# Optimization experiments

Hardware: AMD Instinct MI355X
Metric: run time of the kernel (lower is better)

## Reference

```python
import jax, jax.numpy as jnp
import numpy as np

H = 512          # hidden_size
L = 1024         # total sequence length (q_len + c_len + t_len)
C = 512          # number of columns (key/value length)
NUM_REL = 51     # len(relations2id)


def setup_inputs() -> dict:
    key = jax.random.key(0)
    ks = jax.random.split(key, 12)
    w = 1.0 / np.sqrt(H)  # torch nn.Linear default init scale
    return {
        "query": jax.random.normal(ks[0], (1, L, H), jnp.float32),
        "key": jax.random.normal(ks[1], (1, C, H), jnp.float32),
        "value": jax.random.normal(ks[2], (1, C, H), jnp.float32),
        "predefined_relation": jax.random.randint(ks[3], (L, L), 0, NUM_REL, dtype=jnp.int32),
        "q_len": 384,
        "c_len": 512,
        "Wq": jax.random.uniform(ks[4], (H, H), jnp.float32, -w, w),
        "bq": jnp.zeros((H,), jnp.float32),
        "Wk": jax.random.uniform(ks[5], (H, H), jnp.float32, -w, w),
        "bk": jnp.zeros((H,), jnp.float32),
        "Wv": jax.random.uniform(ks[6], (H, H), jnp.float32, -w, w),
        "bv": jnp.zeros((H,), jnp.float32),
        "rel_k_emb": jax.random.normal(ks[7], (NUM_REL, H), jnp.float32),
        "rel_v_emb": jax.random.normal(ks[8], (NUM_REL, H), jnp.float32),
    }


def reference(query, key, value, predefined_relation, q_len, c_len,
              Wq, bq, Wk, bk, Wv, bv, rel_k_emb, rel_v_emb):
    # --- get_fixed_column_relation (kind='column', enable_latent_relations=False) ---
    # predefined_relation: [L, L] relation ids; take column block [L, C]
    mc = predefined_relation[:, q_len:q_len + c_len]          # [L, C]
    relation_k = rel_k_emb[mc]                                # [L, C, H]
    relation_v = rel_v_emb[mc]                                # [L, C, H] (value path discarded by forward)
    # --- single-head projections (nbatches == 1) ---
    q = query[0] @ Wq.T + bq                                  # [L, H]
    k = key[0] @ Wk.T + bk                                    # [C, H]
    v = value[0] @ Wv.T + bv                                  # [C, H]
    # --- relative_attention_logits ---
    qk = q @ k.T                                              # [L, C]
    q_rel = jnp.einsum('lh,lch->lc', q, relation_k)           # per-query relation scores [L, C]
    scores = (qk + q_rel) / np.sqrt(H).astype(np.float32)
    attn = jax.nn.softmax(scores, axis=-1)                    # [L, C]
    # forward returns self.attn[0, 0] (the pre-dropout attention probabilities);
    # relative_attention_values output (attn @ v + einsum('lc,lch->lh', attn, relation_v))
    # is computed in the torch module but discarded, so we return only attn.
    return attn
```

## Files before the change

### kernel.cpp

```cpp
#include <hip/hip_runtime.h>
#include <hip/hip_bf16.h>

#define HH 512
#define LL 1024
#define CC 512
#define NREL 51

typedef __attribute__((ext_vector_type(8))) short bf16x8;
typedef __attribute__((ext_vector_type(4))) float f32x4;
typedef __attribute__((ext_vector_type(2))) float f32x2;

__device__ __forceinline__ short f2bn(float f) {
    return __builtin_bit_cast(short, __float2bfloat16(f));
}

__device__ __forceinline__ void gl16(const void* g, void* l) {
    __builtin_amdgcn_global_load_lds(
        (const __attribute__((address_space(1))) void*)g,
        (__attribute__((address_space(3))) void*)l, 16, 0, 0);
}

__global__ __launch_bounds__(256) void k1_proj(
    const float* __restrict__ query, const float* __restrict__ key,
    const float* __restrict__ Wq, const float* __restrict__ Wk,
    const float* __restrict__ relk, const float* __restrict__ bq,
    short* __restrict__ qbuf, short* __restrict__ kbuf,
    float* __restrict__ Rpart)
{
    __shared__ __align__(16) short Alds[16 * 512];
    __shared__ __align__(16) short Blds[64 * 512];
    const int b = blockIdx.x, tid = threadIdx.x;
    const int w = tid >> 6, lane = tid & 63;
    const bool isq = (b < 512);
    const float *A, *B; short* outp; int m0, n0;
    if (isq) { A = query; B = Wq; outp = qbuf;
               m0 = (b >> 3) * 16; n0 = (b & 7) * 64; }
    else     { const int bb = b - 512; A = key; B = Wk; outp = kbuf;
               m0 = (bb >> 3) * 16; n0 = (bb & 7) * 64; }

    {
        const int ar = tid >> 4, ac = (tid & 15) * 8;
        #pragma unroll
        for (int j = 0; j < 4; ++j) {
            const int c = ac + j * 128;
            float4 x = *(const float4*)(A + (m0 + ar) * HH + c);
            float4 y = *(const float4*)(A + (m0 + ar) * HH + c + 4);
            bf16x8 o;
            o[0] = f2bn(x.x); o[1] = f2bn(x.y); o[2] = f2bn(x.z); o[3] = f2bn(x.w);
            o[4] = f2bn(y.x); o[5] = f2bn(y.y); o[6] = f2bn(y.z); o[7] = f2bn(y.w);
            *(bf16x8*)(Alds + ar * 512 + (((c >> 3) ^ (ar & 7)) << 3)) = o;
        }
        const int br = tid >> 2, bc = (tid & 3) * 16;
        #pragma unroll
        for (int j = 0; j < 8; ++j) {
            const int c = bc + j * 64;
            float4 x0 = *(const float4*)(B + (n0 + br) * HH + c);
            float4 x1 = *(const float4*)(B + (n0 + br) * HH + c + 4);
            float4 x2 = *(const float4*)(B + (n0 + br) * HH + c + 8);
            float4 x3 = *(const float4*)(B + (n0 + br) * HH + c + 12);
            bf16x8 o0, o1;
            o0[0] = f2bn(x0.x); o0[1] = f2bn(x0.y); o0[2] = f2bn(x0.z); o0[3] = f2bn(x0.w);
            o0[4] = f2bn(x1.x); o0[5] = f2bn(x1.y); o0[6] = f2bn(x1.z); o0[7] = f2bn(x1.w);
            o1[0] = f2bn(x2.x); o1[1] = f2bn(x2.y); o1[2] = f2bn(x2.z); o1[3] = f2bn(x2.w);
            o1[4] = f2bn(x3.x); o1[5] = f2bn(x3.y); o1[6] = f2bn(x3.z); o1[7] = f2bn(x3.w);
            *(bf16x8*)(Blds + br * 512 + ((((c >> 3) + 0) ^ (br & 7)) << 3)) = o0;
            *(bf16x8*)(Blds + br * 512 + ((((c >> 3) + 1) ^ (br & 7)) << 3)) = o1;
        }
    }
    __syncthreads();

    const int lr = lane & 15, lk = (lane >> 4) * 8;
    const int lx = 8 * (lr & 7);
    f32x4 acc[4] = {};
    #pragma unroll
    for (int t = 0; t < 2; ++t) {
        const int k0g = w * 128 + t * 64;
        bf16x8 a0 = *(const bf16x8*)(Alds + lr * 512 + k0g + ((0 + lk) ^ lx));
        bf16x8 a1 = *(const bf16x8*)(Alds + lr * 512 + k0g + ((32 + lk) ^ lx));
        #pragma unroll
        for (int f = 0; f < 4; ++f) {
            const int ro = (f * 16 + lr) * 512 + k0g;
            bf16x8 b0 = *(const bf16x8*)(Blds + ro + ((0 + lk) ^ lx));
            bf16x8 b1 = *(const bf16x8*)(Blds + ro + ((32 + lk) ^ lx));
            acc[f] = __builtin_amdgcn_mfma_f32_16x16x32_bf16(a0, b0, acc[f], 0, 0, 0);
            acc[f] = __builtin_amdgcn_mfma_f32_16x16x32_bf16(a1, b1, acc[f], 0, 0, 0);
        }
    }
    __syncthreads();

    float* P = (float*)Blds;
    if (w) {
        #pragma unroll
        for (int f = 0; f < 4; ++f)
            *(f32x4*)(P + (w - 1) * 1024 + lane * 16 + f * 4) = acc[f];
    }
    __syncthreads();

    short* qt   = Blds + 8192;
    short* Brel = Blds + 16384;
    if (w == 0) {
        #pragma unroll
        for (int wv = 0; wv < 3; ++wv)
            #pragma unroll
            for (int f = 0; f < 4; ++f)
                acc[f] += *(const f32x4*)(P + wv * 1024 + lane * 16 + f * 4);
        #pragma unroll
        for (int f = 0; f < 4; ++f) {
            const int colg = f * 16 + lr;
            const float bv = isq ? bq[n0 + colg] : 0.f;
            #pragma unroll
            for (int r = 0; r < 4; ++r) {
                const int row = (lane >> 4) * 4 + r;
                const short h = f2bn(acc[f][r] + bv);
                outp[(m0 + row) * HH + n0 + (colg ^ (8 * (row & 7)))] = h;
                if (isq)
                    qt[row * 64 + (((colg >> 3) ^ (row & 7)) << 3) + (colg & 7)] = h;
            }
        }
    } else if (isq) {
        for (int i = tid - 64; i < 1024; i += 192) {
            const int rr = i >> 4, c4 = (i & 15) * 4;
            float4 v = make_float4(0.f, 0.f, 0.f, 0.f);
            if (rr < NREL) v = *(const float4*)(relk + rr * HH + n0 + c4);
            short4 o;
            o.x = f2bn(v.x); o.y = f2bn(v.y); o.z = f2bn(v.z); o.w = f2bn(v.w);
            *(short4*)(Brel + rr * 64 + (((c4 >> 3) ^ (rr & 7)) << 3) + (c4 & 7)) = o;
        }
    }
    __syncthreads();

    if (w == 0 && isq) {
        bf16x8 a0 = *(const bf16x8*)(qt + lr * 64 + ((0 + lk) ^ lx));
        bf16x8 a1 = *(const bf16x8*)(qt + lr * 64 + ((32 + lk) ^ lx));
        f32x4 racc[4] = {};
        #pragma unroll
        for (int f = 0; f < 4; ++f) {
            const int ro = (f * 16 + lr) * 64;
            bf16x8 b0 = *(const bf16x8*)(Brel + ro + ((0 + lk) ^ lx));
            bf16x8 b1 = *(const bf16x8*)(Brel + ro + ((32 + lk) ^ lx));
            racc[f] = __builtin_amdgcn_mfma_f32_16x16x32_bf16(a0, b0, racc[f], 0, 0, 0);
            racc[f] = __builtin_amdgcn_mfma_f32_16x16x32_bf16(a1, b1, racc[f], 0, 0, 0);
        }
        #pragma unroll
        for (int f = 0; f < 4; ++f)
            #pragma unroll
            for (int r = 0; r < 4; ++r)
                Rpart[(b & 7) * (LL * 64) + (m0 + (lane >> 4) * 4 + r) * 64 + f * 16 + lr]
                    = racc[f][r];
    }
}

__global__ __launch_bounds__(512) void k2_attn(
    const short* __restrict__ qbuf, const short* __restrict__ kbuf,
    const int* __restrict__ rel, const int* __restrict__ qlen,
    const float* __restrict__ Rpart, float* __restrict__ out)
{
    __shared__ __align__(16) short Bb[8][2][4096];
    __shared__ float Rs[16][64];
    __shared__ float psum[8][16];
    const int b = blockIdx.x, tid = threadIdx.x;
    const int w = tid >> 6, lane = tid & 63;
    const int l0 = b * 16, cb = w * 64;
    const int lr = lane & 15, lk = (lane >> 4) * 8;
    const int lx = 8 * (lr & 7);
    const int srow = lane >> 3, scol = (lane & 7) * 8;
    const int qoff = qlen[0];

    const int rrow = tid >> 5, rc = (tid & 31) * 2;
    f32x2 rpv[8];
    #pragma unroll
    for (int p = 0; p < 8; ++p)
        rpv[p] = *(const f32x2*)(Rpart + p * (LL * 64) + (l0 + rrow) * 64 + rc);
    int idxr[4][4];
    #pragma unroll
    for (int r = 0; r < 4; ++r) {
        const int row = (lane >> 4) * 4 + r;
        #pragma unroll
        for (int f = 0; f < 4; ++f)
            idxr[r][f] = rel[(l0 + row) * LL + qoff + cb + f * 16 + lr];
    }
    __builtin_amdgcn_sched_barrier(0);

    bf16x8 a0v[2], a1v[2];
#define K2_STAGE(bi, t) do { \
        const int k0g = (t) * 64; \
        short* Lb = &Bb[w][bi][0]; \
        _Pragma("unroll") \
        for (int j = 0; j < 8; ++j) \
            gl16(kbuf + (cb + j * 8 + srow) * HH + k0g + scol, Lb + j * 512); \
        a0v[bi] = *(const bf16x8*)(qbuf + (l0 + lr) * HH + k0g + ((0 + lk) ^ lx)); \
        a1v[bi] = *(const bf16x8*)(qbuf + (l0 + lr) * HH + k0g + ((32 + lk) ^ lx)); \
    } while (0)

    f32x4 acc[4] = {};
#define K2_COMP(bi) do { \
        const short* Lb = &Bb[w][bi][0]; \
        _Pragma("unroll") \
        for (int f = 0; f < 4; ++f) { \
            const int ro = (f * 16 + lr) * 64; \
            bf16x8 k0f = *(const bf16x8*)(Lb + ro + ((0 + lk) ^ lx)); \
            bf16x8 k1f = *(const bf16x8*)(Lb + ro + ((32 + lk) ^ lx)); \
            acc[f] = __builtin_amdgcn_mfma_f32_16x16x32_bf16(a0v[bi], k0f, acc[f], 0, 0, 0); \
            acc[f] = __builtin_amdgcn_mfma_f32_16x16x32_bf16(a1v[bi], k1f, acc[f], 0, 0, 0); \
        } \
    } while (0)

    K2_STAGE(0, 0);
    #pragma unroll
    for (int t = 0; t < 8; ++t) {
        if (t < 7) {
            K2_STAGE((t + 1) & 1, t + 1);
            asm volatile("s_waitcnt vmcnt(10)" ::: "memory");
        } else {
            asm volatile("s_waitcnt vmcnt(0)" ::: "memory");
        }
        __builtin_amdgcn_sched_barrier(0);
        K2_COMP(t & 1);
    }
#undef K2_STAGE
#undef K2_COMP

    float rx = 0.f, ry = 0.f;
    #pragma unroll
    for (int p = 0; p < 8; ++p) { rx += rpv[p][0]; ry += rpv[p][1]; }
    Rs[rrow][rc] = rx; Rs[rrow][rc + 1] = ry;
    __syncthreads();

    const float scale = 0.04419417382415922f;
    #pragma unroll
    for (int r = 0; r < 4; ++r) {
        const int row = (lane >> 4) * 4 + r;
        float s = 0.f;
        #pragma unroll
        for (int f = 0; f < 4; ++f) {
            float e = __expf((acc[f][r] + Rs[row][idxr[r][f]]) * scale);
            acc[f][r] = e; s += e;
        }
        #pragma unroll
        for (int sh = 1; sh < 16; sh <<= 1) s += __shfl_xor(s, sh, 64);
        if (lr == 0) psum[w][row] = s;
    }
    __syncthreads();
    #pragma unroll
    for (int r = 0; r < 4; ++r) {
        const int row = (lane >> 4) * 4 + r;
        float tot = 0.f;
        #pragma unroll
        for (int wv = 0; wv < 8; ++wv) tot += psum[wv][row];
        const float inv = 1.f / tot;
        #pragma unroll
        for (int f = 0; f < 4; ++f)
            out[(l0 + row) * CC + cb + f * 16 + lr] = acc[f][r] * inv;
    }
}

extern "C" void kernel_launch(void* const* d_in, const int* in_sizes, int n_in,
                              void* d_out, int out_size, void* d_ws, size_t ws_size,
                              hipStream_t stream) {
    const float* query = (const float*)d_in[0];
    const float* key   = (const float*)d_in[1];
    const int*   rel   = (const int*)d_in[3];
    const int*   qlen  = (const int*)d_in[4];
    const float* Wq    = (const float*)d_in[6];
    const float* bq    = (const float*)d_in[7];
    const float* Wk    = (const float*)d_in[8];
    const float* relk  = (const float*)d_in[12];

    float* out = (float*)d_out;
    short* p = (short*)d_ws;
    short* qbuf  = p;  p += LL * HH;
    short* kbuf  = p;  p += CC * HH;
    float* Rpart = (float*)p;

    k1_proj<<<768, 256, 0, stream>>>(query, key, Wq, Wk, relk, bq,
                                     qbuf, kbuf, Rpart);
    k2_attn<<<64, 512, 0, stream>>>(qbuf, kbuf, rel, qlen, Rpart, out);
}
```

Baseline: 27.75 us.

## Retile projection GEMM, move relation-score GEMM into attention kernel

The projection kernel now uses 64-row tiles with 512 threads. Each block stages only the weight tile in LDS and streams the activation rows straight from global memory, which shrinks the grid from 768 blocks to 193. The q·relk relation-score product moves out of the projection kernel into the attention kernel, using a pre-converted bf16 relk table written by one extra block. This removes the Rpart partial-sum buffer and its global round trip. The attention kernel also drops its LDS staging of K via global_load_lds and uses a 3-deep register prefetch of K fragments instead, trading LDS traffic for more register pressure and uncoalesced global reads.

Result: faster. 27.19 us (-2.0%).

```diff
diff --git a/kernel.cpp b/kernel.cpp
--- a/kernel.cpp
+++ b/kernel.cpp
@@ -8,75 +8,67 @@
 
 typedef __attribute__((ext_vector_type(8))) short bf16x8;
 typedef __attribute__((ext_vector_type(4))) float f32x4;
-typedef __attribute__((ext_vector_type(2))) float f32x2;
 
 __device__ __forceinline__ short f2bn(float f) {
     return __builtin_bit_cast(short, __float2bfloat16(f));
 }
 
-__device__ __forceinline__ void gl16(const void* g, void* l) {
-    __builtin_amdgcn_global_load_lds(
-        (const __attribute__((address_space(1))) void*)g,
-        (__attribute__((address_space(3))) void*)l, 16, 0, 0);
-}
-
-__global__ __launch_bounds__(256) void k1_proj(
+__device__ __forceinline__ bf16x8 cvt8(const float* p) {
+    float4 x = *(const float4*)p;
+    float4 y = *(const float4*)(p + 4);
+    bf16x8 o;
+    o[0] = f2bn(x.x); o[1] = f2bn(x.y); o[2] = f2bn(x.z); o[3] = f2bn(x.w);
+    o[4] = f2bn(y.x); o[5] = f2bn(y.y); o[6] = f2bn(y.z); o[7] = f2bn(y.w);
+    return o;
+}
+
+__global__ __launch_bounds__(512) void k1_proj(
     const float* __restrict__ query, const float* __restrict__ key,
     const float* __restrict__ Wq, const float* __restrict__ Wk,
     const float* __restrict__ relk, const float* __restrict__ bq,
     short* __restrict__ qbuf, short* __restrict__ kbuf,
-    float* __restrict__ Rpart)
+    short* __restrict__ relkb)
 {
-    __shared__ __align__(16) short Alds[16 * 512];
+    const int b = blockIdx.x, tid = threadIdx.x;
+    if (b == 192) {
+        for (int i = tid; i < 64 * 64; i += 512) {
+            const int rr = i >> 6, c8 = i & 63;
+            bf16x8 o = {};
+            if (rr < NREL) o = cvt8(relk + rr * HH + c8 * 8);
+            *(bf16x8*)(relkb + rr * HH + ((c8 ^ (rr & 7)) << 3)) = o;
+        }
+        return;
+    }
     __shared__ __align__(16) short Blds[64 * 512];
-    const int b = blockIdx.x, tid = threadIdx.x;
     const int w = tid >> 6, lane = tid & 63;
-    const bool isq = (b < 512);
+    const int ms = w >> 1, ks = w & 1;
+    const bool isq = (b < 128);
     const float *A, *B; short* outp; int m0, n0;
     if (isq) { A = query; B = Wq; outp = qbuf;
-               m0 = (b >> 3) * 16; n0 = (b & 7) * 64; }
-    else     { const int bb = b - 512; A = key; B = Wk; outp = kbuf;
-               m0 = (bb >> 3) * 16; n0 = (bb & 7) * 64; }
+               m0 = (b >> 3) * 64; n0 = (b & 7) * 64; }
+    else     { const int bb = b - 128; A = key; B = Wk; outp = kbuf;
+               m0 = (bb >> 3) * 64; n0 = (bb & 7) * 64; }
 
     {
-        const int ar = tid >> 4, ac = (tid & 15) * 8;
-        #pragma unroll
-        for (int j = 0; j < 4; ++j) {
-            const int c = ac + j * 128;
-            float4 x = *(const float4*)(A + (m0 + ar) * HH + c);
-            float4 y = *(const float4*)(A + (m0 + ar) * HH + c + 4);
-            bf16x8 o;
-            o[0] = f2bn(x.x); o[1] = f2bn(x.y); o[2] = f2bn(x.z); o[3] = f2bn(x.w);
-            o[4] = f2bn(y.x); o[5] = f2bn(y.y); o[6] = f2bn(y.z); o[7] = f2bn(y.w);
-            *(bf16x8*)(Alds + ar * 512 + (((c >> 3) ^ (ar & 7)) << 3)) = o;
-        }
-        const int br = tid >> 2, bc = (tid & 3) * 16;
+        const int br = tid >> 3, cbase = tid & 7;
         #pragma unroll
         for (int j = 0; j < 8; ++j) {
-            const int c = bc + j * 64;
-            float4 x0 = *(const float4*)(B + (n0 + br) * HH + c);
-            float4 x1 = *(const float4*)(B + (n0 + br) * HH + c + 4);
-            float4 x2 = *(const float4*)(B + (n0 + br) * HH + c + 8);
-            float4 x3 = *(const float4*)(B + (n0 + br) * HH + c + 12);
-            bf16x8 o0, o1;
-            o0[0] = f2bn(x0.x); o0[1] = f2bn(x0.y); o0[2] = f2bn(x0.z); o0[3] = f2bn(x0.w);
-            o0[4] = f2bn(x1.x); o0[5] = f2bn(x1.y); o0[6] = f2bn(x1.z); o0[7] = f2bn(x1.w);
-            o1[0] = f2bn(x2.x); o1[1] = f2bn(x2.y); o1[2] = f2bn(x2.z); o1[3] = f2bn(x2.w);
-            o1[4] = f2bn(x3.x); o1[5] = f2bn(x3.y); o1[6] = f2bn(x3.z); o1[7] = f2bn(x3.w);
-            *(bf16x8*)(Blds + br * 512 + ((((c >> 3) + 0) ^ (br & 7)) << 3)) = o0;
-            *(bf16x8*)(Blds + br * 512 + ((((c >> 3) + 1) ^ (br & 7)) << 3)) = o1;
+            const int c8 = cbase + j * 8;
+            bf16x8 o = cvt8(B + (n0 + br) * HH + c8 * 8);
+            *(bf16x8*)(Blds + br * 512 + ((c8 ^ (br & 7)) << 3)) = o;
         }
     }
     __syncthreads();
 
     const int lr = lane & 15, lk = (lane >> 4) * 8;
     const int lx = 8 * (lr & 7);
+    const int arow = m0 + ms * 16 + lr;
     f32x4 acc[4] = {};
     #pragma unroll
-    for (int t = 0; t < 2; ++t) {
-        const int k0g = w * 128 + t * 64;
-        bf16x8 a0 = *(const bf16x8*)(Alds + lr * 512 + k0g + ((0 + lk) ^ lx));
-        bf16x8 a1 = *(const bf16x8*)(Alds + lr * 512 + k0g + ((32 + lk) ^ lx));
+    for (int t = 0; t < 4; ++t) {
+        const int k0g = ks * 256 + t * 64;
+        bf16x8 a0 = cvt8(A + arow * HH + k0g + lk);
+        bf16x8 a1 = cvt8(A + arow * HH + k0g + 32 + lk);
         #pragma unroll
         for (int f = 0; f < 4; ++f) {
             const int ro = (f * 16 + lr) * 512 + k0g;
@@ -87,75 +79,37 @@
         }
     }
     __syncthreads();
-
     float* P = (float*)Blds;
-    if (w) {
-        #pragma unroll
-        for (int f = 0; f < 4; ++f)
-            *(f32x4*)(P + (w - 1) * 1024 + lane * 16 + f * 4) = acc[f];
-    }
-    __syncthreads();
-
-    short* qt   = Blds + 8192;
-    short* Brel = Blds + 16384;
-    if (w == 0) {
-        #pragma unroll
-        for (int wv = 0; wv < 3; ++wv)
-            #pragma unroll
-            for (int f = 0; f < 4; ++f)
-                acc[f] += *(const f32x4*)(P + wv * 1024 + lane * 16 + f * 4);
+    if (ks) {
+        #pragma unroll
+        for (int f = 0; f < 4; ++f)
+            *(f32x4*)(P + (ms * 64 + lane) * 16 + f * 4) = acc[f];
+    }
+    __syncthreads();
+    if (!ks) {
+        #pragma unroll
+        for (int f = 0; f < 4; ++f)
+            acc[f] += *(const f32x4*)(P + (ms * 64 + lane) * 16 + f * 4);
         #pragma unroll
         for (int f = 0; f < 4; ++f) {
             const int colg = f * 16 + lr;
             const float bv = isq ? bq[n0 + colg] : 0.f;
             #pragma unroll
             for (int r = 0; r < 4; ++r) {
-                const int row = (lane >> 4) * 4 + r;
-                const short h = f2bn(acc[f][r] + bv);
-                outp[(m0 + row) * HH + n0 + (colg ^ (8 * (row & 7)))] = h;
-                if (isq)
-                    qt[row * 64 + (((colg >> 3) ^ (row & 7)) << 3) + (colg & 7)] = h;
+                const int row = ms * 16 + (lane >> 4) * 4 + r;
+                outp[(m0 + row) * HH + n0 + (colg ^ (8 * (row & 7)))]
+                    = f2bn(acc[f][r] + bv);
             }
         }
-    } else if (isq) {
-        for (int i = tid - 64; i < 1024; i += 192) {
-            const int rr = i >> 4, c4 = (i & 15) * 4;
-            float4 v = make_float4(0.f, 0.f, 0.f, 0.f);
-            if (rr < NREL) v = *(const float4*)(relk + rr * HH + n0 + c4);
-            short4 o;
-            o.x = f2bn(v.x); o.y = f2bn(v.y); o.z = f2bn(v.z); o.w = f2bn(v.w);
-            *(short4*)(Brel + rr * 64 + (((c4 >> 3) ^ (rr & 7)) << 3) + (c4 & 7)) = o;
-        }
-    }
-    __syncthreads();
-
-    if (w == 0 && isq) {
-        bf16x8 a0 = *(const bf16x8*)(qt + lr * 64 + ((0 + lk) ^ lx));
-        bf16x8 a1 = *(const bf16x8*)(qt + lr * 64 + ((32 + lk) ^ lx));
-        f32x4 racc[4] = {};
-        #pragma unroll
-        for (int f = 0; f < 4; ++f) {
-            const int ro = (f * 16 + lr) * 64;
-            bf16x8 b0 = *(const bf16x8*)(Brel + ro + ((0 + lk) ^ lx));
-            bf16x8 b1 = *(const bf16x8*)(Brel + ro + ((32 + lk) ^ lx));
-            racc[f] = __builtin_amdgcn_mfma_f32_16x16x32_bf16(a0, b0, racc[f], 0, 0, 0);
-            racc[f] = __builtin_amdgcn_mfma_f32_16x16x32_bf16(a1, b1, racc[f], 0, 0, 0);
-        }
-        #pragma unroll
-        for (int f = 0; f < 4; ++f)
-            #pragma unroll
-            for (int r = 0; r < 4; ++r)
-                Rpart[(b & 7) * (LL * 64) + (m0 + (lane >> 4) * 4 + r) * 64 + f * 16 + lr]
-                    = racc[f][r];
     }
 }
 
 __global__ __launch_bounds__(512) void k2_attn(
     const short* __restrict__ qbuf, const short* __restrict__ kbuf,
-    const int* __restrict__ rel, const int* __restrict__ qlen,
-    const float* __restrict__ Rpart, float* __restrict__ out)
+    const short* __restrict__ relkb, const int* __restrict__ rel,
+    const int* __restrict__ qlen, float* __restrict__ out)
 {
-    __shared__ __align__(16) short Bb[8][2][4096];
+    __shared__ float Rpark[8][16][64];
     __shared__ float Rs[16][64];
     __shared__ float psum[8][16];
     const int b = blockIdx.x, tid = threadIdx.x;
@@ -163,14 +117,8 @@
     const int l0 = b * 16, cb = w * 64;
     const int lr = lane & 15, lk = (lane >> 4) * 8;
     const int lx = 8 * (lr & 7);
-    const int srow = lane >> 3, scol = (lane & 7) * 8;
     const int qoff = qlen[0];
 
-    const int rrow = tid >> 5, rc = (tid & 31) * 2;
-    f32x2 rpv[8];
-    #pragma unroll
-    for (int p = 0; p < 8; ++p)
-        rpv[p] = *(const f32x2*)(Rpart + p * (LL * 64) + (l0 + rrow) * 64 + rc);
     int idxr[4][4];
     #pragma unroll
     for (int r = 0; r < 4; ++r) {
@@ -179,51 +127,62 @@
         for (int f = 0; f < 4; ++f)
             idxr[r][f] = rel[(l0 + row) * LL + qoff + cb + f * 16 + lr];
     }
-    __builtin_amdgcn_sched_barrier(0);
-
-    bf16x8 a0v[2], a1v[2];
-#define K2_STAGE(bi, t) do { \
+
+    f32x4 acc[4] = {};
+    bf16x8 a0v[3], a1v[3], kbv[3][8];
+#define K2_LOAD(bi, t) do { \
         const int k0g = (t) * 64; \
-        short* Lb = &Bb[w][bi][0]; \
-        _Pragma("unroll") \
-        for (int j = 0; j < 8; ++j) \
-            gl16(kbuf + (cb + j * 8 + srow) * HH + k0g + scol, Lb + j * 512); \
         a0v[bi] = *(const bf16x8*)(qbuf + (l0 + lr) * HH + k0g + ((0 + lk) ^ lx)); \
         a1v[bi] = *(const bf16x8*)(qbuf + (l0 + lr) * HH + k0g + ((32 + lk) ^ lx)); \
-    } while (0)
-
-    f32x4 acc[4] = {};
-#define K2_COMP(bi) do { \
-        const short* Lb = &Bb[w][bi][0]; \
         _Pragma("unroll") \
         for (int f = 0; f < 4; ++f) { \
-            const int ro = (f * 16 + lr) * 64; \
-            bf16x8 k0f = *(const bf16x8*)(Lb + ro + ((0 + lk) ^ lx)); \
-            bf16x8 k1f = *(const bf16x8*)(Lb + ro + ((32 + lk) ^ lx)); \
-            acc[f] = __builtin_amdgcn_mfma_f32_16x16x32_bf16(a0v[bi], k0f, acc[f], 0, 0, 0); \
-            acc[f] = __builtin_amdgcn_mfma_f32_16x16x32_bf16(a1v[bi], k1f, acc[f], 0, 0, 0); \
-        } \
-    } while (0)
-
-    K2_STAGE(0, 0);
+            kbv[bi][2*f]   = *(const bf16x8*)(kbuf + (cb + f*16 + lr) * HH + k0g + ((0 + lk) ^ lx)); \
+            kbv[bi][2*f+1] = *(const bf16x8*)(kbuf + (cb + f*16 + lr) * HH + k0g + ((32 + lk) ^ lx)); \
+        } } while (0)
+#define K2_COMP(bi) do { \
+        _Pragma("unroll") \
+        for (int f = 0; f < 4; ++f) { \
+            acc[f] = __builtin_amdgcn_mfma_f32_16x16x32_bf16(a0v[bi], kbv[bi][2*f],   acc[f], 0, 0, 0); \
+            acc[f] = __builtin_amdgcn_mfma_f32_16x16x32_bf16(a1v[bi], kbv[bi][2*f+1], acc[f], 0, 0, 0); \
+        } } while (0)
+
+    K2_LOAD(0, 0); K2_LOAD(1, 1);
     #pragma unroll
     for (int t = 0; t < 8; ++t) {
-        if (t < 7) {
-            K2_STAGE((t + 1) & 1, t + 1);
-            asm volatile("s_waitcnt vmcnt(10)" ::: "memory");
-        } else {
-            asm volatile("s_waitcnt vmcnt(0)" ::: "memory");
-        }
-        __builtin_amdgcn_sched_barrier(0);
-        K2_COMP(t & 1);
-    }
-#undef K2_STAGE
+        if (t < 6) K2_LOAD((t + 2) % 3, t + 2);
+        K2_COMP(t % 3);
+    }
+#undef K2_LOAD
 #undef K2_COMP
 
-    float rx = 0.f, ry = 0.f;
-    #pragma unroll
-    for (int p = 0; p < 8; ++p) { rx += rpv[p][0]; ry += rpv[p][1]; }
-    Rs[rrow][rc] = rx; Rs[rrow][rc + 1] = ry;
+    {
+        const int k0g = w * 64;
+        bf16x8 a0 = *(const bf16x8*)(qbuf + (l0 + lr) * HH + k0g + ((0 + lk) ^ lx));
+        bf16x8 a1 = *(const bf16x8*)(qbuf + (l0 + lr) * HH + k0g + ((32 + lk) ^ lx));
+        f32x4 racc[4] = {};
+        #pragma unroll
+        for (int f = 0; f < 4; ++f) {
+            const int ro = (f * 16 + lr) * HH + k0g;
+            bf16x8 b0 = *(const bf16x8*)(relkb + ro + ((0 + lk) ^ lx));
+            bf16x8 b1 = *(const bf16x8*)(relkb + ro + ((32 + lk) ^ lx));
+            racc[f] = __builtin_amdgcn_mfma_f32_16x16x32_bf16(a0, b0, racc[f], 0, 0, 0);
+            racc[f] = __builtin_amdgcn_mfma_f32_16x16x32_bf16(a1, b1, racc[f], 0, 0, 0);
+        }
+        #pragma unroll
+        for (int f = 0; f < 4; ++f)
+            #pragma unroll
+            for (int r = 0; r < 4; ++r)
+                Rpark[w][(lane >> 4) * 4 + r][f * 16 + lr] = racc[f][r];
+    }
+    __syncthreads();
+    #pragma unroll
+    for (int rr = 0; rr < 2; ++rr) {
+        const int row = w * 2 + rr;
+        float s = 0.f;
+        #pragma unroll
+        for (int pp = 0; pp < 8; ++pp) s += Rpark[pp][row][lane];
+        Rs[row][lane] = s;
+    }
     __syncthreads();
 
     const float scale = 0.04419417382415922f;
@@ -270,9 +229,9 @@
     short* p = (short*)d_ws;
     short* qbuf  = p;  p += LL * HH;
     short* kbuf  = p;  p += CC * HH;
-    float* Rpart = (float*)p;
-
-    k1_proj<<<768, 256, 0, stream>>>(query, key, Wq, Wk, relk, bq,
-                                     qbuf, kbuf, Rpart);
-    k2_attn<<<64, 512, 0, stream>>>(qbuf, kbuf, rel, qlen, Rpart, out);
-}
+    short* relkb = p;  p += 64 * HH;
+
+    k1_proj<<<193, 512, 0, stream>>>(query, key, Wq, Wk, relk, bq,
+                                     qbuf, kbuf, relkb);
+    k2_attn<<<64, 512, 0, stream>>>(qbuf, kbuf, relkb, rel, qlen, out);
+}
```
